# Optimization experiments

Hardware: AMD Instinct MI355X
Metric: run time of the kernel (lower is better)

Reference implementation:

```python
import jax, jax.numpy as jnp
import numpy as np

V, D, DI, DS, DC, DTR, L, H, BS, B, T = 32000, 512, 1024, 16, 4, 32, 4, 2048, 1024, 2, 1024


def layer_norm(x, g, b):
    m = jnp.mean(x, axis=-1, keepdims=True)
    v = jnp.mean(jnp.square(x - m), axis=-1, keepdims=True)
    return (x - m) * jax.lax.rsqrt(v + 1e-5) * g + b


def mamba(x, p):
    # x: [B, T, D]
    Bb = x.shape[0]
    xz = jnp.einsum('btd,ed->bte', x, p['W_in'])          # [B,T,2*DI]
    u, z = jnp.split(xz, 2, axis=-1)
    # causal depthwise conv over time
    uc = jnp.transpose(u, (0, 2, 1))                       # [B,DI,T]
    uc = jax.lax.conv_general_dilated(uc, p['conv_w'][:, None, :], (1,), [(DC - 1, 0)], feature_group_count=DI)
    uc = uc + p['conv_b'][None, :, None]
    u = jax.nn.silu(jnp.transpose(uc, (0, 2, 1)))          # [B,T,DI]
    x_dbl = jnp.einsum('btd,ed->bte', u, p['W_xp'])        # [B,T,DTR+2*DS]
    dt = jax.nn.softplus(jnp.einsum('btr,dr->btd', x_dbl[..., :DTR], p['W_dt']) + p['b_dt'])  # [B,T,DI]
    Bm = x_dbl[..., DTR:DTR + DS]                          # [B,T,DS]
    Cm = x_dbl[..., DTR + DS:]                             # [B,T,DS]
    A = -jnp.exp(p['A_log'])                               # [DI,DS]

    def step(h, inp):
        dt_t, B_t, C_t, u_t = inp                          # [B,DI],[B,DS],[B,DS],[B,DI]
        dA = jnp.exp(dt_t[:, :, None] * A)                 # [B,DI,DS]
        h = dA * h + (dt_t * u_t)[:, :, None] * B_t[:, None, :]
        return h, jnp.einsum('bds,bs->bd', h, C_t)

    h0 = jnp.zeros((Bb, DI, DS), x.dtype)
    _, ys = jax.lax.scan(step, h0, (dt.transpose(1, 0, 2), Bm.transpose(1, 0, 2), Cm.transpose(1, 0, 2), u.transpose(1, 0, 2)))
    y = ys.transpose(1, 0, 2) + u * p['D_p']               # skip term D*u
    y = y * jax.nn.silu(z)
    return jnp.einsum('bte,de->btd', y, p['W_out'])


def setup_inputs() -> dict:
    key = jax.random.key(0)
    ks = jax.random.split(key, 16)
    s = 0.02
    rn = lambda k, sh: (jax.random.normal(k, sh, jnp.float32) * s)
    inp = {
        'idx': jax.random.randint(ks[0], (B, T), 0, V),
        'tok_emb': rn(ks[1], (V, D)),
        'pos_emb': rn(ks[2], (BS, D)),
        'ln1_g': jnp.ones((L, D), jnp.float32), 'ln1_b': jnp.zeros((L, D), jnp.float32),
        'W_in': rn(ks[3], (L, 2 * DI, D)),
        'conv_w': rn(ks[4], (L, DI, DC)), 'conv_b': jnp.zeros((L, DI), jnp.float32),
        'W_xp': rn(ks[5], (L, DTR + 2 * DS, DI)),
        'W_dt': rn(ks[6], (L, DI, DTR)), 'b_dt': jnp.full((L, DI), -4.6, jnp.float32),
        'A_log': jnp.tile(jnp.log(jnp.arange(1, DS + 1, dtype=jnp.float32))[None, None, :], (L, DI, 1)),
        'D_p': jnp.ones((L, DI), jnp.float32),
        'W_out': rn(ks[7], (L, D, DI)),
        'ln2_g': jnp.ones((L, D), jnp.float32), 'ln2_b': jnp.zeros((L, D), jnp.float32),
        'W_f1': rn(ks[8], (L, H, D)), 'b_f1': jnp.zeros((L, H), jnp.float32),
        'W_f2': rn(ks[9], (L, D, H)), 'b_f2': jnp.zeros((L, D), jnp.float32),
        'lm_w': rn(ks[10], (V, D)), 'lm_b': jnp.zeros((V,), jnp.float32),
    }
    return inp


def reference(idx, tok_emb, pos_emb, ln1_g, ln1_b, W_in, conv_w, conv_b, W_xp, W_dt, b_dt, A_log, D_p, W_out, ln2_g, ln2_b, W_f1, b_f1, W_f2, b_f2, lm_w, lm_b):
    x = tok_emb[idx] + pos_emb[:idx.shape[1]]              # [B,T,D]
    layers = {'ln1_g': ln1_g, 'ln1_b': ln1_b, 'W_in': W_in, 'conv_w': conv_w, 'conv_b': conv_b,
              'W_xp': W_xp, 'W_dt': W_dt, 'b_dt': b_dt, 'A_log': A_log, 'D_p': D_p, 'W_out': W_out,
              'ln2_g': ln2_g, 'ln2_b': ln2_b, 'W_f1': W_f1, 'b_f1': b_f1, 'W_f2': W_f2, 'b_f2': b_f2}

    def blk(x, p):
        x = x + mamba(layer_norm(x, p['ln1_g'], p['ln1_b']), p)
        h = layer_norm(x, p['ln2_g'], p['ln2_b'])
        h = jax.nn.relu(jnp.einsum('btd,hd->bth', h, p['W_f1']) + p['b_f1'])
        x = x + jnp.einsum('bth,dh->btd', h, p['W_f2']) + p['b_f2']
        return x, None

    x, _ = jax.lax.scan(blk, x, layers)
    logits = jnp.einsum('btd,vd->btv', x, lm_w) + lm_b     # [B,T,V]
    return logits
```

## Files before the change

### kernel.cpp

```cpp
#include <hip/hip_runtime.h>
#include <cstdint>
#include <cstddef>

typedef __bf16 bf16;
typedef __bf16 bf16x8 __attribute__((ext_vector_type(8)));
typedef __bf16 bf16x4 __attribute__((ext_vector_type(4)));
typedef float  f32x4  __attribute__((ext_vector_type(4)));

#define D_MODEL 512
#define D_INNER 1024
#define D_STATE 16
#define D_CONV  4
#define DT_RANK 32
#define N_LAYER 4
#define H_FFN   2048
#define SEQ_T   1024
#define BATCH   2
#define BT      (BATCH * SEQ_T)
#define VOCAB   32000

#define NCHUNK  16
#define CHUNK   (SEQ_T / NCHUNK)

__device__ __forceinline__ float b2f(bf16 x) { return (float)x; }
__device__ __forceinline__ bf16  f2b(float x) { return (bf16)x; }

__device__ __forceinline__ float rdf(const void* p, long i, int bf) {
  return bf ? (float)((const bf16*)p)[i] : ((const float*)p)[i];
}

__device__ __forceinline__ void async16(const void* g, void* l) {
  __builtin_amdgcn_global_load_lds((const __attribute__((address_space(1))) void*)g,
                                   (__attribute__((address_space(3))) void*)l, 16, 0, 0);
}

__global__ void probe_k(const unsigned short* __restrict__ tok,
                        const unsigned short* __restrict__ pos,
                        int* __restrict__ flag)
{
  int lane = threadIdx.x;
  int bad = 0;
  for (int i = lane; i < 512; i += 64) {
    int e0 = (tok[i] >> 7) & 0xFF;
    int e1 = (pos[i] >> 7) & 0xFF;
    if (e0 >= 134 || e1 >= 134) bad = 1;
  }
  unsigned long long m = __ballot(bad);
  if (lane == 0) *flag = (m == 0ULL) ? 1 : 0;
}

__global__ __launch_bounds__(256) void cvt_k(const float4* __restrict__ src,
                                             bf16* __restrict__ dst,
                                             int n4, const int* __restrict__ dflag)
{
  if (*dflag) return;
  int i = blockIdx.x * 256 + threadIdx.x;
  if (i >= n4) return;
  float4 v = src[i];
  bf16x4 o; o[0] = f2b(v.x); o[1] = f2b(v.y); o[2] = f2b(v.z); o[3] = f2b(v.w);
  *(bf16x4*)(dst + (size_t)i * 4) = o;
}

template<int OUTMODE, bool RELU>
__global__ __launch_bounds__(256) void gemm_nt(
    const bf16* __restrict__ A, const bf16* __restrict__ Barena,
    const void* __restrict__ Braw, long boff,
    void* __restrict__ Cout, const void* __restrict__ bias, long biasoff,
    const float* __restrict__ res, const int* __restrict__ dflag,
    int M, int N, int K)
{
  __shared__ __attribute__((aligned(16))) bf16 As[128 * 32];
  __shared__ __attribute__((aligned(16))) bf16 Bs[128 * 32];

  const int bf = *dflag;
  const bf16* Bw = bf ? ((const bf16*)Braw + boff) : Barena;

  const int tid  = threadIdx.x;
  const int lane = tid & 63;
  const int q    = lane >> 4;
  const int m16  = lane & 15;
  const int w    = tid >> 6;
  const int wr   = w >> 1, wc = w & 1;

  const int rowA0 = blockIdx.y * 128;
  const int rowB0 = blockIdx.x * 128;

  f32x4 acc[4][4] = {};

  for (int k0 = 0; k0 < K; k0 += 32) {
#pragma unroll
    for (int r = 0; r < 2; r++) {
      int ci  = r * 256 + tid;
      int row = ci >> 2;
      int kc  = ci & 3;
      const bf16* ga = A  + (size_t)(rowA0 + row) * K + (k0 + kc * 8);
      const bf16* gb = Bw + (size_t)(rowB0 + row) * K + (k0 + kc * 8);
      char* la = (char*)As + (size_t)(r * 256 + (tid & 192)) * 16;
      char* lb = (char*)Bs + (size_t)(r * 256 + (tid & 192)) * 16;
      async16(ga, la);
      async16(gb, lb);
    }
    __syncthreads();

    bf16x8 af[4], bfr[4];
#pragma unroll
    for (int mt = 0; mt < 4; mt++)
      af[mt] = *(const bf16x8*)&As[(wr * 64 + mt * 16 + m16) * 32 + q * 8];
#pragma unroll
    for (int nt = 0; nt < 4; nt++)
      bfr[nt] = *(const bf16x8*)&Bs[(wc * 64 + nt * 16 + m16) * 32 + q * 8];

#pragma unroll
    for (int mt = 0; mt < 4; mt++)
#pragma unroll
      for (int nt = 0; nt < 4; nt++)
        acc[mt][nt] = __builtin_amdgcn_mfma_f32_16x16x32_bf16(
            af[mt], bfr[nt], acc[mt][nt], 0, 0, 0);

    __syncthreads();
  }

#pragma unroll
  for (int mt = 0; mt < 4; mt++) {
#pragma unroll
    for (int r = 0; r < 4; r++) {
      int row = rowA0 + wr * 64 + mt * 16 + q * 4 + r;
#pragma unroll
      for (int nt = 0; nt < 4; nt++) {
        int col = rowB0 + wc * 64 + nt * 16 + m16;
        float v = acc[mt][nt][r];
        if (bias) v += rdf(bias, biasoff + col, bf);
        if (res)  v += res[(size_t)row * N + col];
        if (RELU) v = fmaxf(v, 0.f);
        size_t oi = (size_t)row * N + col;
        if (OUTMODE == 1 || (OUTMODE == 2 && bf)) ((bf16*)Cout)[oi] = f2b(v);
        else                                      ((float*)Cout)[oi] = v;
      }
    }
  }
}

__global__ void embed_k(const int* __restrict__ idx, const void* __restrict__ tok,
                        const void* __restrict__ pos, float* __restrict__ x,
                        const int* __restrict__ dflag)
{
  int bf = *dflag;
  int bt = blockIdx.x;
  int t  = bt & (SEQ_T - 1);
  long rowv = idx[bt];
  for (int i = threadIdx.x; i < D_MODEL; i += blockDim.x)
    x[(size_t)bt * D_MODEL + i] = rdf(tok, rowv * D_MODEL + i, bf)
                                + rdf(pos, (long)t * D_MODEL + i, bf);
}

__global__ __launch_bounds__(64) void ln_k(const float* __restrict__ x,
                                           const void* __restrict__ g,
                                           const void* __restrict__ bb,
                                           long goff,
                                           bf16* __restrict__ out,
                                           const int* __restrict__ dflag)
{
  int bf = *dflag;
  int row = blockIdx.x;
  const float4* xr = (const float4*)(x + (size_t)row * D_MODEL);
  int l = threadIdx.x;
  float4 v0 = xr[l];
  float4 v1 = xr[64 + l];
  float s  = (v0.x + v0.y) + (v0.z + v0.w) + (v1.x + v1.y) + (v1.z + v1.w);
  float ss = v0.x*v0.x + v0.y*v0.y + v0.z*v0.z + v0.w*v0.w
           + v1.x*v1.x + v1.y*v1.y + v1.z*v1.z + v1.w*v1.w;
#pragma unroll
  for (int o = 32; o; o >>= 1) { s += __shfl_xor(s, o); ss += __shfl_xor(ss, o); }
  float m   = s  * (1.f / 512.f);
  float var = ss * (1.f / 512.f) - m * m;
  float inv = rsqrtf(var + 1e-5f);
  float vs[8] = {v0.x, v0.y, v0.z, v0.w, v1.x, v1.y, v1.z, v1.w};
  int i0 = l * 4, i1 = 256 + l * 4;
#pragma unroll
  for (int e = 0; e < 4; e++) {
    out[(size_t)row * D_MODEL + i0 + e] =
        f2b((vs[e] - m) * inv * rdf(g, goff + i0 + e, bf) + rdf(bb, goff + i0 + e, bf));
    out[(size_t)row * D_MODEL + i1 + e] =
        f2b((vs[4 + e] - m) * inv * rdf(g, goff + i1 + e, bf) + rdf(bb, goff + i1 + e, bf));
  }
}

__global__ __launch_bounds__(256) void conv_silu_k(const float* __restrict__ xz,
                                                   const void* __restrict__ cw,
                                                   const void* __restrict__ cb,
                                                   long cwoff, long cboff,
                                                   bf16* __restrict__ u,
                                                   const int* __restrict__ dflag)
{
  int bf  = *dflag;
  int gid = blockIdx.x * 256 + threadIdx.x;
  int d   = gid & (D_INNER - 1);
  int bt  = gid >> 10;
  int t   = bt & (SEQ_T - 1);
  float acc = rdf(cb, cboff + d, bf);
#pragma unroll
  for (int k = 0; k < D_CONV; k++) {
    int tt = t + k - (D_CONV - 1);
    if (tt >= 0)
      acc += xz[(size_t)(bt + k - (D_CONV - 1)) * (2 * D_INNER) + d]
           * rdf(cw, cwoff + (long)d * D_CONV + k, bf);
  }
  float sig = 1.f / (1.f + __expf(-acc));
  u[gid] = f2b(acc * sig);
}

__global__ __launch_bounds__(256) void xdbl_k(const bf16* __restrict__ u,
                                              const bf16* __restrict__ Warena,
                                              const void* __restrict__ Wraw, long woff,
                                              float* __restrict__ xd,
                                              const int* __restrict__ dflag)
{
  int bf = *dflag;
  const bf16* Wxp = bf ? ((const bf16*)Wraw + woff) : Warena;
  int t = blockIdx.x;
  __shared__ float us[D_INNER];
  __shared__ float red[256];
  for (int i = threadIdx.x; i < D_INNER; i += 256)
    us[i] = b2f(u[(size_t)t * D_INNER + i]);
  __syncthreads();
  int j = threadIdx.x >> 2, p = threadIdx.x & 3;
  const bf16x8* wr = (const bf16x8*)(Wxp + (size_t)j * D_INNER + p * 256);
  float s = 0.f;
#pragma unroll 4
  for (int c = 0; c < 32; c++) {
    bf16x8 wv = wr[c];
    int k = p * 256 + c * 8;
#pragma unroll
    for (int e = 0; e < 8; e++) s += us[k + e] * b2f(wv[e]);
  }
  red[threadIdx.x] = s;
  __syncthreads();
  if (p == 0)
    xd[(size_t)t * 64 + j] = red[threadIdx.x] + red[threadIdx.x + 1]
                           + red[threadIdx.x + 2] + red[threadIdx.x + 3];
}

__global__ __launch_bounds__(256) void dt_k(const float* __restrict__ xd,
                                            const bf16* __restrict__ Warena,
                                            const void* __restrict__ Wraw, long woff,
                                            const void* __restrict__ bdt, long boff,
                                            float* __restrict__ dtb,
                                            const int* __restrict__ dflag)
{
  int bf = *dflag;
  const bf16* Wdt = bf ? ((const bf16*)Wraw + woff) : Warena;
  int t = blockIdx.x >> 2;
  int d = ((blockIdx.x & 3) << 8) + threadIdx.x;
  __shared__ float xr[DT_RANK];
  if (threadIdx.x < DT_RANK) xr[threadIdx.x] = xd[(size_t)t * 64 + threadIdx.x];
  __syncthreads();
  float s = rdf(bdt, boff + d, bf);
  const bf16x8* wr = (const bf16x8*)(Wdt + (size_t)d * DT_RANK);
#pragma unroll
  for (int c = 0; c < 4; c++) {
    bf16x8 wv = wr[c];
#pragma unroll
    for (int e = 0; e < 8; e++) s += xr[c * 8 + e] * b2f(wv[e]);
  }
  s = (s > 20.f) ? s : log1pf(__expf(s));
  dtb[(size_t)t * D_INNER + d] = s;
}

__global__ __launch_bounds__(256) void scanA_k(const float* __restrict__ dtb,
                                               const bf16* __restrict__ u,
                                               const float* __restrict__ xd,
                                               const void* __restrict__ A_log, long aoff,
                                               float* __restrict__ Pb,
                                               float* __restrict__ Qb,
                                               const int* __restrict__ dflag)
{
  int bf = *dflag;
  int s  = threadIdx.x & 15;
  int dl = threadIdx.x >> 4;
  int c  = blockIdx.x & (NCHUNK - 1);
  int dg = (blockIdx.x >> 4) & 63;
  int b  = blockIdx.x >> 10;
  int d  = dg * 16 + dl;

  float Av = -__expf(rdf(A_log, aoff + (long)d * D_STATE + s, bf));
  float h = 0.f, P = 1.f;
  size_t row0 = (size_t)b * SEQ_T + (size_t)c * CHUNK;

  float dt_n = dtb[row0 * D_INNER + d];
  float u_n  = b2f(u[row0 * D_INNER + d]);
  float B_n  = xd[row0 * 64 + DT_RANK + s];

  for (int t = 0; t < CHUNK; t++) {
    float dt_v = dt_n, u_v = u_n, Bv = B_n;
    if (t + 1 < CHUNK) {
      size_t r1 = row0 + t + 1;
      dt_n = dtb[r1 * D_INNER + d];
      u_n  = b2f(u[r1 * D_INNER + d]);
      B_n  = xd[r1 * 64 + DT_RANK + s];
    }
    float dA = __expf(dt_v * Av);
    P *= dA;
    h = dA * h + (dt_v * u_v) * Bv;
  }
  size_t o = (((size_t)b * D_INNER + d) * D_STATE + s) * NCHUNK + c;
  Pb[o] = P;
  Qb[o] = h;
}

__global__ __launch_bounds__(256) void scanB_k(const float* __restrict__ Pb,
                                               const float* __restrict__ Qb,
                                               float* __restrict__ Hin)
{
  int tid = blockIdx.x * 256 + threadIdx.x;
  size_t base = (size_t)tid * NCHUNK;
  float h = 0.f;
#pragma unroll
  for (int c = 0; c < NCHUNK; c++) {
    Hin[base + c] = h;
    h = Pb[base + c] * h + Qb[base + c];
  }
}

__global__ __launch_bounds__(256) void scanC_k(const float* __restrict__ dtb,
                                               const bf16* __restrict__ u,
                                               const float* __restrict__ xd,
                                               const float* __restrict__ xz,
                                               const void* __restrict__ A_log, long aoff,
                                               const void* __restrict__ D_p, long doff,
                                               const float* __restrict__ Hin,
                                               bf16* __restrict__ y,
                                               const int* __restrict__ dflag)
{
  int bf = *dflag;
  int s  = threadIdx.x & 15;
  int dl = threadIdx.x >> 4;
  int c  = blockIdx.x & (NCHUNK - 1);
  int dg = (blockIdx.x >> 4) & 63;
  int b  = blockIdx.x >> 10;
  int d  = dg * 16 + dl;

  float Av = -__expf(rdf(A_log, aoff + (long)d * D_STATE + s, bf));
  float Dv = rdf(D_p, doff + d, bf);
  float h  = Hin[(((size_t)b * D_INNER + d) * D_STATE + s) * NCHUNK + c];
  size_t row0 = (size_t)b * SEQ_T + (size_t)c * CHUNK;

  float dt_n = dtb[row0 * D_INNER + d];
  float u_n  = b2f(u[row0 * D_INNER + d]);
  float B_n  = xd[row0 * 64 + DT_RANK + s];
  float C_n  = xd[row0 * 64 + DT_RANK + D_STATE + s];

  for (int t = 0; t < CHUNK; t++) {
    float dt_v = dt_n, u_v = u_n, Bv = B_n, Cv = C_n;
    if (t + 1 < CHUNK) {
      size_t r1 = row0 + t + 1;
      dt_n = dtb[r1 * D_INNER + d];
      u_n  = b2f(u[r1 * D_INNER + d]);
      B_n  = xd[r1 * 64 + DT_RANK + s];
      C_n  = xd[r1 * 64 + DT_RANK + D_STATE + s];
    }
    float dA = __expf(dt_v * Av);
    h = dA * h + (dt_v * u_v) * Bv;
    float p = h * Cv;
    p += __shfl_xor(p, 1);
    p += __shfl_xor(p, 2);
    p += __shfl_xor(p, 4);
    p += __shfl_xor(p, 8);
    if (s == 0) {
      size_t r = row0 + t;
      float zv  = xz[r * (2 * D_INNER) + D_INNER + d];
      float sig = 1.f / (1.f + __expf(-zv));
      y[r * D_INNER + d] = f2b((p + u_v * Dv) * (zv * sig));
    }
  }
}

__global__ void cast_k(const float* __restrict__ x, bf16* __restrict__ o, int n)
{
  int i = blockIdx.x * 256 + threadIdx.x;
  if (i < n) o[i] = f2b(x[i]);
}

extern "C" void kernel_launch(void* const* d_in, const int* in_sizes, int n_in,
                              void* d_out, int out_size, void* d_ws, size_t ws_size,
                              hipStream_t stream)
{
  const int* idx = (const int*)d_in[0];
  const void* tok    = d_in[1];
  const void* pos    = d_in[2];
  const void* ln1_g  = d_in[3];
  const void* ln1_b  = d_in[4];
  const void* W_in   = d_in[5];
  const void* conv_w = d_in[6];
  const void* conv_b = d_in[7];
  const void* W_xp   = d_in[8];
  const void* W_dt   = d_in[9];
  const void* b_dt   = d_in[10];
  const void* A_log  = d_in[11];
  const void* D_p    = d_in[12];
  const void* W_out  = d_in[13];
  const void* ln2_g  = d_in[14];
  const void* ln2_b  = d_in[15];
  const void* W_f1   = d_in[16];
  const void* b_f1   = d_in[17];
  const void* W_f2   = d_in[18];
  const void* b_f2   = d_in[19];
  const void* lm_w   = d_in[20];
  const void* lm_b   = d_in[21];

  char* ws = (char*)d_ws;
  int*  dflag = (int*)ws;    ws += 256;
  float* x_res = (float*)ws; ws += (size_t)BT * D_MODEL * 4;
  float* xz    = (float*)ws; ws += (size_t)BT * 2 * D_INNER * 4;
  float* xdbl  = (float*)ws; ws += (size_t)BT * 64 * 4;
  float* dtb   = (float*)ws; ws += (size_t)BT * D_INNER * 4;
  bf16* lnbuf  = (bf16*)ws;  ws += (size_t)BT * D_MODEL * 2;
  bf16* ubuf   = (bf16*)ws;  ws += (size_t)BT * D_INNER * 2;
  bf16* ybuf   = (bf16*)ws;  ws += (size_t)BT * D_INNER * 2;
  bf16* hbuf   = (bf16*)ws;  ws += (size_t)BT * H_FFN * 2;
  float* Pbuf  = (float*)ws; ws += (size_t)BATCH * D_INNER * D_STATE * NCHUNK * 4;
  float* Qbuf  = (float*)ws; ws += (size_t)BATCH * D_INNER * D_STATE * NCHUNK * 4;
  float* Hin   = (float*)ws; ws += (size_t)BATCH * D_INNER * D_STATE * NCHUNK * 4;
  bf16* aW_in  = (bf16*)ws;  ws += (size_t)N_LAYER * 2*D_INNER * D_MODEL * 2;
  bf16* aW_xp  = (bf16*)ws;  ws += (size_t)N_LAYER * 64 * D_INNER * 2;
  bf16* aW_dt  = (bf16*)ws;  ws += (size_t)N_LAYER * D_INNER * DT_RANK * 2;
  bf16* aW_out = (bf16*)ws;  ws += (size_t)N_LAYER * D_MODEL * D_INNER * 2;
  bf16* aW_f1  = (bf16*)ws;  ws += (size_t)N_LAYER * H_FFN * D_MODEL * 2;
  bf16* aW_f2  = (bf16*)ws;  ws += (size_t)N_LAYER * D_MODEL * H_FFN * 2;
  bf16* aLm    = (bf16*)ws;  ws += (size_t)VOCAB * D_MODEL * 2;

  probe_k<<<1, 64, 0, stream>>>((const unsigned short*)tok,
                                (const unsigned short*)pos, dflag);

  auto cvt = [&](const void* src, bf16* dst, long n) {
    int n4 = (int)(n / 4);
    cvt_k<<<(n4 + 255) / 256, 256, 0, stream>>>((const float4*)src, dst, n4, dflag);
  };
  cvt(W_in,  aW_in,  (long)N_LAYER * 2*D_INNER * D_MODEL);
  cvt(W_xp,  aW_xp,  (long)N_LAYER * 64 * D_INNER);
  cvt(W_dt,  aW_dt,  (long)N_LAYER * D_INNER * DT_RANK);
  cvt(W_out, aW_out, (long)N_LAYER * D_MODEL * D_INNER);
  cvt(W_f1,  aW_f1,  (long)N_LAYER * H_FFN * D_MODEL);
  cvt(W_f2,  aW_f2,  (long)N_LAYER * D_MODEL * H_FFN);
  cvt(lm_w,  aLm,    (long)VOCAB * D_MODEL);

  embed_k<<<BT, 256, 0, stream>>>(idx, tok, pos, x_res, dflag);

  for (int l = 0; l < N_LAYER; l++) {
    long oWin = (long)l * 2*D_INNER * D_MODEL;
    long oWxp = (long)l * 64 * D_INNER;
    long oWdt = (long)l * D_INNER * DT_RANK;
    long oWo  = (long)l * D_MODEL * D_INNER;
    long oWf1 = (long)l * H_FFN * D_MODEL;
    long oWf2 = (long)l * D_MODEL * H_FFN;
    long oA   = (long)l * D_INNER * D_STATE;
    long oD   = (long)l * D_INNER;

    ln_k<<<BT, 64, 0, stream>>>(x_res, ln1_g, ln1_b, (long)l * D_MODEL, lnbuf, dflag);

    gemm_nt<0, false><<<dim3(2 * D_INNER / 128, BT / 128), 256, 0, stream>>>(
        lnbuf, aW_in + oWin, W_in, oWin, xz, nullptr, 0, nullptr, dflag,
        BT, 2 * D_INNER, D_MODEL);

    conv_silu_k<<<BT * D_INNER / 256, 256, 0, stream>>>(
        xz, conv_w, conv_b, (long)l * D_INNER * D_CONV, oD, ubuf, dflag);

    xdbl_k<<<BT, 256, 0, stream>>>(ubuf, aW_xp + oWxp, W_xp, oWxp, xdbl, dflag);

    dt_k<<<BT * 4, 256, 0, stream>>>(
        xdbl, aW_dt + oWdt, W_dt, oWdt, b_dt, oD, dtb, dflag);

    scanA_k<<<BATCH * 64 * NCHUNK, 256, 0, stream>>>(
        dtb, ubuf, xdbl, A_log, oA, Pbuf, Qbuf, dflag);
    scanB_k<<<BATCH * D_INNER * D_STATE / 256, 256, 0, stream>>>(Pbuf, Qbuf, Hin);
    scanC_k<<<BATCH * 64 * NCHUNK, 256, 0, stream>>>(
        dtb, ubuf, xdbl, xz, A_log, oA, D_p, oD, Hin, ybuf, dflag);

    gemm_nt<0, false><<<dim3(D_MODEL / 128, BT / 128), 256, 0, stream>>>(
        ybuf, aW_out + oWo, W_out, oWo, x_res, nullptr, 0, x_res, dflag,
        BT, D_MODEL, D_INNER);

    ln_k<<<BT, 64, 0, stream>>>(x_res, ln2_g, ln2_b, (long)l * D_MODEL, lnbuf, dflag);

    gemm_nt<1, true><<<dim3(H_FFN / 128, BT / 128), 256, 0, stream>>>(
        lnbuf, aW_f1 + oWf1, W_f1, oWf1, hbuf, b_f1, (long)l * H_FFN, nullptr, dflag,
        BT, H_FFN, D_MODEL);

    gemm_nt<0, false><<<dim3(D_MODEL / 128, BT / 128), 256, 0, stream>>>(
        hbuf, aW_f2 + oWf2, W_f2, oWf2, x_res, b_f2, (long)l * D_MODEL, x_res, dflag,
        BT, D_MODEL, H_FFN);
  }

  cast_k<<<BT * D_MODEL / 256, 256, 0, stream>>>(x_res, lnbuf, BT * D_MODEL);

  gemm_nt<2, false><<<dim3(VOCAB / 128, BT / 128), 256, 0, stream>>>(
      lnbuf, aLm, lm_w, 0, d_out, lm_b, 0, nullptr, dflag,
      BT, VOCAB, D_MODEL);
}
```

Before: 1.760 ms.

## Triple-buffer GEMM K-loop, swizzle LM-head blocks, vectorize xdbl input load

The GEMM main loop moves from one LDS tile per step to a 3-slot ring. Loads are issued two tiles ahead, and vmcnt/lgkmcnt waits with raw barriers replace __syncthreads, so global-to-LDS copies overlap the MFMA work. The LM-head GEMM also remaps block IDs so that consecutive blocks share the same N tile, which is meant to improve L2 reuse of lm_w. In xdbl_k the u row is loaded with 8-wide vector loads. The extra slots triple LDS use and may lower occupancy, and the hand-written wait counts must match the number of async loads per stage. The wraparound prefetch in the final iterations reloads tiles that are never used.

```diff
diff --git a/kernel.cpp b/kernel.cpp
--- a/kernel.cpp
+++ b/kernel.cpp
@@ -61,7 +61,7 @@
   *(bf16x4*)(dst + (size_t)i * 4) = o;
 }
 
-template<int OUTMODE, bool RELU>
+template<int OUTMODE, bool RELU, bool SWZ>
 __global__ __launch_bounds__(256) void gemm_nt(
     const bf16* __restrict__ A, const bf16* __restrict__ Barena,
     const void* __restrict__ Braw, long boff,
@@ -69,8 +69,8 @@
     const float* __restrict__ res, const int* __restrict__ dflag,
     int M, int N, int K)
 {
-  __shared__ __attribute__((aligned(16))) bf16 As[128 * 32];
-  __shared__ __attribute__((aligned(16))) bf16 Bs[128 * 32];
+  __shared__ __attribute__((aligned(16))) bf16 As[3][128 * 32];
+  __shared__ __attribute__((aligned(16))) bf16 Bs[3][128 * 32];
 
   const int bf = *dflag;
   const bf16* Bw = bf ? ((const bf16*)Braw + boff) : Barena;
@@ -82,12 +82,27 @@
   const int w    = tid >> 6;
   const int wr   = w >> 1, wc = w & 1;
 
-  const int rowA0 = blockIdx.y * 128;
-  const int rowB0 = blockIdx.x * 128;
+  int bx = blockIdx.x, by = blockIdx.y;
+  if (SWZ) {
+    int gx = gridDim.x, gy = gridDim.y;
+    int n  = gx * gy;
+    if ((n & 7) == 0) {
+      int id  = by * gx + bx;
+      int nid = (id & 7) * (n >> 3) + (id >> 3);
+      bx = nid / gy;
+      by = nid % gy;
+    }
+  }
+
+  const int rowA0 = by * 128;
+  const int rowB0 = bx * 128;
 
   f32x4 acc[4][4] = {};
 
-  for (int k0 = 0; k0 < K; k0 += 32) {
+  const int NT = K >> 5;
+
+  auto stage = [&](int slot, int kt) {
+    int k0 = kt << 5;
 #pragma unroll
     for (int r = 0; r < 2; r++) {
       int ci  = r * 256 + tid;
@@ -95,20 +110,35 @@
       int kc  = ci & 3;
       const bf16* ga = A  + (size_t)(rowA0 + row) * K + (k0 + kc * 8);
       const bf16* gb = Bw + (size_t)(rowB0 + row) * K + (k0 + kc * 8);
-      char* la = (char*)As + (size_t)(r * 256 + (tid & 192)) * 16;
-      char* lb = (char*)Bs + (size_t)(r * 256 + (tid & 192)) * 16;
+      char* la = (char*)&As[slot][0] + (size_t)(r * 256 + (tid & 192)) * 16;
+      char* lb = (char*)&Bs[slot][0] + (size_t)(r * 256 + (tid & 192)) * 16;
       async16(ga, la);
       async16(gb, lb);
     }
-    __syncthreads();
-
+  };
+
+  stage(0, 0);
+  stage(1, 1 < NT ? 1 : 0);
+
+  for (int t = 0; t < NT; t++) {
+    int t2 = t + 2; if (t2 >= NT) t2 -= NT;
+    stage((t + 2) % 3, t2);
+
+    asm volatile("s_waitcnt vmcnt(8)" ::: "memory");
+    __builtin_amdgcn_s_barrier();
+
+    const int sl = t % 3;
     bf16x8 af[4], bfr[4];
 #pragma unroll
     for (int mt = 0; mt < 4; mt++)
-      af[mt] = *(const bf16x8*)&As[(wr * 64 + mt * 16 + m16) * 32 + q * 8];
+      af[mt] = *(const bf16x8*)&As[sl][(wr * 64 + mt * 16 + m16) * 32 + q * 8];
 #pragma unroll
     for (int nt = 0; nt < 4; nt++)
-      bfr[nt] = *(const bf16x8*)&Bs[(wc * 64 + nt * 16 + m16) * 32 + q * 8];
+      bfr[nt] = *(const bf16x8*)&Bs[sl][(wc * 64 + nt * 16 + m16) * 32 + q * 8];
+
+    asm volatile("s_waitcnt lgkmcnt(0)" ::: "memory");
+    __builtin_amdgcn_sched_barrier(0);
+    __builtin_amdgcn_s_barrier();
 
 #pragma unroll
     for (int mt = 0; mt < 4; mt++)
@@ -116,9 +146,9 @@
       for (int nt = 0; nt < 4; nt++)
         acc[mt][nt] = __builtin_amdgcn_mfma_f32_16x16x32_bf16(
             af[mt], bfr[nt], acc[mt][nt], 0, 0, 0);
-
-    __syncthreads();
-  }
+  }
+
+  asm volatile("s_waitcnt vmcnt(0)" ::: "memory");
 
 #pragma unroll
   for (int mt = 0; mt < 4; mt++) {
@@ -220,8 +250,11 @@
   int t = blockIdx.x;
   __shared__ float us[D_INNER];
   __shared__ float red[256];
-  for (int i = threadIdx.x; i < D_INNER; i += 256)
-    us[i] = b2f(u[(size_t)t * D_INNER + i]);
+  if (threadIdx.x < D_INNER / 8) {
+    bf16x8 v = *(const bf16x8*)(u + (size_t)t * D_INNER + threadIdx.x * 8);
+#pragma unroll
+    for (int e = 0; e < 8; e++) us[threadIdx.x * 8 + e] = b2f(v[e]);
+  }
   __syncthreads();
   int j = threadIdx.x >> 2, p = threadIdx.x & 3;
   const bf16x8* wr = (const bf16x8*)(Wxp + (size_t)j * D_INNER + p * 256);
@@ -457,7 +490,7 @@
 
     ln_k<<<BT, 64, 0, stream>>>(x_res, ln1_g, ln1_b, (long)l * D_MODEL, lnbuf, dflag);
 
-    gemm_nt<0, false><<<dim3(2 * D_INNER / 128, BT / 128), 256, 0, stream>>>(
+    gemm_nt<0, false, false><<<dim3(2 * D_INNER / 128, BT / 128), 256, 0, stream>>>(
         lnbuf, aW_in + oWin, W_in, oWin, xz, nullptr, 0, nullptr, dflag,
         BT, 2 * D_INNER, D_MODEL);
 
@@ -475,24 +508,24 @@
     scanC_k<<<BATCH * 64 * NCHUNK, 256, 0, stream>>>(
         dtb, ubuf, xdbl, xz, A_log, oA, D_p, oD, Hin, ybuf, dflag);
 
-    gemm_nt<0, false><<<dim3(D_MODEL / 128, BT / 128), 256, 0, stream>>>(
+    gemm_nt<0, false, false><<<dim3(D_MODEL / 128, BT / 128), 256, 0, stream>>>(
         ybuf, aW_out + oWo, W_out, oWo, x_res, nullptr, 0, x_res, dflag,
         BT, D_MODEL, D_INNER);
 
     ln_k<<<BT, 64, 0, stream>>>(x_res, ln2_g, ln2_b, (long)l * D_MODEL, lnbuf, dflag);
 
-    gemm_nt<1, true><<<dim3(H_FFN / 128, BT / 128), 256, 0, stream>>>(
+    gemm_nt<1, true, false><<<dim3(H_FFN / 128, BT / 128), 256, 0, stream>>>(
         lnbuf, aW_f1 + oWf1, W_f1, oWf1, hbuf, b_f1, (long)l * H_FFN, nullptr, dflag,
         BT, H_FFN, D_MODEL);
 
-    gemm_nt<0, false><<<dim3(D_MODEL / 128, BT / 128), 256, 0, stream>>>(
+    gemm_nt<0, false, false><<<dim3(D_MODEL / 128, BT / 128), 256, 0, stream>>>(
         hbuf, aW_f2 + oWf2, W_f2, oWf2, x_res, b_f2, (long)l * D_MODEL, x_res, dflag,
         BT, D_MODEL, H_FFN);
   }
 
   cast_k<<<BT * D_MODEL / 256, 256, 0, stream>>>(x_res, lnbuf, BT * D_MODEL);
 
-  gemm_nt<2, false><<<dim3(VOCAB / 128, BT / 128), 256, 0, stream>>>(
+  gemm_nt<2, false, true><<<dim3(VOCAB / 128, BT / 128), 256, 0, stream>>>(
       lnbuf, aLm, lm_w, 0, d_out, lm_b, 0, nullptr, dflag,
       BT, VOCAB, D_MODEL);
 }
```

Measured after the change: 1.840 ms. 1.05x slower.

## Split-K the narrow residual GEMMs and swizzle the LM-head GEMM grid

Applied to the files above, without the earlier changes.

The out-projection and FFN2 GEMMs (N=512) only launched 64 workgroups. They now run a 4-way split-K kernel that writes fp32 partial sums, followed by a vectorized reduction kernel that adds bias and residual. This spreads the work across far more CUs, at the cost of extra partial-buffer traffic and one more launch per GEMM. The LM-head GEMM is split into two column halves with a block-index swizzle for cache locality, and the xdbl kernel loads its input row as vectors of 8 bf16.

```diff
diff --git a/kernel.cpp b/kernel.cpp
--- a/kernel.cpp
+++ b/kernel.cpp
@@ -22,6 +22,8 @@
 #define NCHUNK  16
 #define CHUNK   (SEQ_T / NCHUNK)
 
+#define KSPLIT  4
+
 __device__ __forceinline__ float b2f(bf16 x) { return (float)x; }
 __device__ __forceinline__ bf16  f2b(float x) { return (bf16)x; }
 
@@ -61,13 +63,13 @@
   *(bf16x4*)(dst + (size_t)i * 4) = o;
 }
 
-template<int OUTMODE, bool RELU>
+template<int OUTMODE, bool RELU, bool SWZ>
 __global__ __launch_bounds__(256) void gemm_nt(
     const bf16* __restrict__ A, const bf16* __restrict__ Barena,
     const void* __restrict__ Braw, long boff,
     void* __restrict__ Cout, const void* __restrict__ bias, long biasoff,
     const float* __restrict__ res, const int* __restrict__ dflag,
-    int M, int N, int K)
+    int M, int N, int K, int ldc, int col0)
 {
   __shared__ __attribute__((aligned(16))) bf16 As[128 * 32];
   __shared__ __attribute__((aligned(16))) bf16 Bs[128 * 32];
@@ -82,8 +84,20 @@
   const int w    = tid >> 6;
   const int wr   = w >> 1, wc = w & 1;
 
-  const int rowA0 = blockIdx.y * 128;
-  const int rowB0 = blockIdx.x * 128;
+  int bx = blockIdx.x, by = blockIdx.y;
+  if (SWZ) {
+    int gx = gridDim.x, gy = gridDim.y;
+    int n  = gx * gy;
+    if ((n & 7) == 0) {
+      int id  = by * gx + bx;
+      int nid = (id & 7) * (n >> 3) + (id >> 3);
+      bx = nid / gy;
+      by = nid % gy;
+    }
+  }
+
+  const int rowA0 = by * 128;
+  const int rowB0 = bx * 128;
 
   f32x4 acc[4][4] = {};
 
@@ -127,17 +141,120 @@
       int row = rowA0 + wr * 64 + mt * 16 + q * 4 + r;
 #pragma unroll
       for (int nt = 0; nt < 4; nt++) {
-        int col = rowB0 + wc * 64 + nt * 16 + m16;
+        int col = col0 + rowB0 + wc * 64 + nt * 16 + m16;
         float v = acc[mt][nt][r];
         if (bias) v += rdf(bias, biasoff + col, bf);
-        if (res)  v += res[(size_t)row * N + col];
+        if (res)  v += res[(size_t)row * ldc + col];
         if (RELU) v = fmaxf(v, 0.f);
-        size_t oi = (size_t)row * N + col;
+        size_t oi = (size_t)row * ldc + col;
         if (OUTMODE == 1 || (OUTMODE == 2 && bf)) ((bf16*)Cout)[oi] = f2b(v);
         else                                      ((float*)Cout)[oi] = v;
       }
     }
   }
+}
+
+__global__ __launch_bounds__(256) void gemm_nt_sk(
+    const bf16* __restrict__ A, const bf16* __restrict__ Barena,
+    const void* __restrict__ Braw, long boff,
+    float* __restrict__ Cpart, const int* __restrict__ dflag,
+    int M, int N, int K)
+{
+  __shared__ __attribute__((aligned(16))) bf16 As[128 * 32];
+  __shared__ __attribute__((aligned(16))) bf16 Bs[128 * 32];
+
+  const int bf = *dflag;
+  const bf16* Bw = bf ? ((const bf16*)Braw + boff) : Barena;
+
+  const int tid  = threadIdx.x;
+  const int lane = tid & 63;
+  const int q    = lane >> 4;
+  const int m16  = lane & 15;
+  const int w    = tid >> 6;
+  const int wr   = w >> 1, wc = w & 1;
+
+  const int rowA0 = blockIdx.y * 128;
+  const int rowB0 = blockIdx.x * 128;
+  const int ks    = blockIdx.z;
+  const int kBeg  = ks * (K / KSPLIT);
+  const int kEnd  = kBeg + (K / KSPLIT);
+
+  f32x4 acc[4][4] = {};
+
+  for (int k0 = kBeg; k0 < kEnd; k0 += 32) {
+#pragma unroll
+    for (int r = 0; r < 2; r++) {
+      int ci  = r * 256 + tid;
+      int row = ci >> 2;
+      int kc  = ci & 3;
+      const bf16* ga = A  + (size_t)(rowA0 + row) * K + (k0 + kc * 8);
+      const bf16* gb = Bw + (size_t)(rowB0 + row) * K + (k0 + kc * 8);
+      char* la = (char*)As + (size_t)(r * 256 + (tid & 192)) * 16;
+      char* lb = (char*)Bs + (size_t)(r * 256 + (tid & 192)) * 16;
+      async16(ga, la);
+      async16(gb, lb);
+    }
+    __syncthreads();
+
+    bf16x8 af[4], bfr[4];
+#pragma unroll
+    for (int mt = 0; mt < 4; mt++)
+      af[mt] = *(const bf16x8*)&As[(wr * 64 + mt * 16 + m16) * 32 + q * 8];
+#pragma unroll
+    for (int nt = 0; nt < 4; nt++)
+      bfr[nt] = *(const bf16x8*)&Bs[(wc * 64 + nt * 16 + m16) * 32 + q * 8];
+
+#pragma unroll
+    for (int mt = 0; mt < 4; mt++)
+#pragma unroll
+      for (int nt = 0; nt < 4; nt++)
+        acc[mt][nt] = __builtin_amdgcn_mfma_f32_16x16x32_bf16(
+            af[mt], bfr[nt], acc[mt][nt], 0, 0, 0);
+
+    __syncthreads();
+  }
+
+#pragma unroll
+  for (int mt = 0; mt < 4; mt++) {
+#pragma unroll
+    for (int r = 0; r < 4; r++) {
+      int row = rowA0 + wr * 64 + mt * 16 + q * 4 + r;
+#pragma unroll
+      for (int nt = 0; nt < 4; nt++) {
+        int col = rowB0 + wc * 64 + nt * 16 + m16;
+        Cpart[((size_t)ks * M + row) * N + col] = acc[mt][nt][r];
+      }
+    }
+  }
+}
+
+__global__ __launch_bounds__(256) void redk_k(const float* __restrict__ part,
+                                              const void* __restrict__ bias, long biasoff,
+                                              const float* __restrict__ res,
+                                              float* __restrict__ out,
+                                              int n, int N, const int* __restrict__ dflag)
+{
+  int bf = *dflag;
+  int i = blockIdx.x * 256 + threadIdx.x;
+  if (i >= n) return;
+  f32x4 s = ((const f32x4*)part)[i];
+#pragma unroll
+  for (int ks = 1; ks < KSPLIT; ks++) {
+    f32x4 p = ((const f32x4*)part)[(size_t)ks * n + i];
+    s.x += p.x; s.y += p.y; s.z += p.z; s.w += p.w;
+  }
+  if (bias) {
+    int col = (i * 4) & (N - 1);
+    s.x += rdf(bias, biasoff + col,     bf);
+    s.y += rdf(bias, biasoff + col + 1, bf);
+    s.z += rdf(bias, biasoff + col + 2, bf);
+    s.w += rdf(bias, biasoff + col + 3, bf);
+  }
+  if (res) {
+    f32x4 r = ((const f32x4*)res)[i];
+    s.x += r.x; s.y += r.y; s.z += r.z; s.w += r.w;
+  }
+  ((f32x4*)out)[i] = s;
 }
 
 __global__ void embed_k(const int* __restrict__ idx, const void* __restrict__ tok,
@@ -220,8 +337,11 @@
   int t = blockIdx.x;
   __shared__ float us[D_INNER];
   __shared__ float red[256];
-  for (int i = threadIdx.x; i < D_INNER; i += 256)
-    us[i] = b2f(u[(size_t)t * D_INNER + i]);
+  if (threadIdx.x < D_INNER / 8) {
+    bf16x8 v = *(const bf16x8*)(u + (size_t)t * D_INNER + threadIdx.x * 8);
+#pragma unroll
+    for (int e = 0; e < 8; e++) us[threadIdx.x * 8 + e] = b2f(v[e]);
+  }
   __syncthreads();
   int j = threadIdx.x >> 2, p = threadIdx.x & 3;
   const bf16x8* wr = (const bf16x8*)(Wxp + (size_t)j * D_INNER + p * 256);
@@ -417,6 +537,7 @@
   bf16* ubuf   = (bf16*)ws;  ws += (size_t)BT * D_INNER * 2;
   bf16* ybuf   = (bf16*)ws;  ws += (size_t)BT * D_INNER * 2;
   bf16* hbuf   = (bf16*)ws;  ws += (size_t)BT * H_FFN * 2;
+  float* cpart = (float*)ws; ws += (size_t)KSPLIT * BT * D_MODEL * 4;
   float* Pbuf  = (float*)ws; ws += (size_t)BATCH * D_INNER * D_STATE * NCHUNK * 4;
   float* Qbuf  = (float*)ws; ws += (size_t)BATCH * D_INNER * D_STATE * NCHUNK * 4;
   float* Hin   = (float*)ws; ws += (size_t)BATCH * D_INNER * D_STATE * NCHUNK * 4;
@@ -457,9 +578,9 @@
 
     ln_k<<<BT, 64, 0, stream>>>(x_res, ln1_g, ln1_b, (long)l * D_MODEL, lnbuf, dflag);
 
-    gemm_nt<0, false><<<dim3(2 * D_INNER / 128, BT / 128), 256, 0, stream>>>(
+    gemm_nt<0, false, false><<<dim3(2 * D_INNER / 128, BT / 128), 256, 0, stream>>>(
         lnbuf, aW_in + oWin, W_in, oWin, xz, nullptr, 0, nullptr, dflag,
-        BT, 2 * D_INNER, D_MODEL);
+        BT, 2 * D_INNER, D_MODEL, 2 * D_INNER, 0);
 
     conv_silu_k<<<BT * D_INNER / 256, 256, 0, stream>>>(
         xz, conv_w, conv_b, (long)l * D_INNER * D_CONV, oD, ubuf, dflag);
@@ -475,24 +596,30 @@
     scanC_k<<<BATCH * 64 * NCHUNK, 256, 0, stream>>>(
         dtb, ubuf, xdbl, xz, A_log, oA, D_p, oD, Hin, ybuf, dflag);
 
-    gemm_nt<0, false><<<dim3(D_MODEL / 128, BT / 128), 256, 0, stream>>>(
-        ybuf, aW_out + oWo, W_out, oWo, x_res, nullptr, 0, x_res, dflag,
-        BT, D_MODEL, D_INNER);
+    gemm_nt_sk<<<dim3(D_MODEL / 128, BT / 128, KSPLIT), 256, 0, stream>>>(
+        ybuf, aW_out + oWo, W_out, oWo, cpart, dflag, BT, D_MODEL, D_INNER);
+    redk_k<<<(BT * D_MODEL / 4 + 255) / 256, 256, 0, stream>>>(
+        cpart, nullptr, 0, x_res, x_res, BT * D_MODEL / 4, D_MODEL, dflag);
 
     ln_k<<<BT, 64, 0, stream>>>(x_res, ln2_g, ln2_b, (long)l * D_MODEL, lnbuf, dflag);
 
-    gemm_nt<1, true><<<dim3(H_FFN / 128, BT / 128), 256, 0, stream>>>(
+    gemm_nt<1, true, false><<<dim3(H_FFN / 128, BT / 128), 256, 0, stream>>>(
         lnbuf, aW_f1 + oWf1, W_f1, oWf1, hbuf, b_f1, (long)l * H_FFN, nullptr, dflag,
-        BT, H_FFN, D_MODEL);
-
-    gemm_nt<0, false><<<dim3(D_MODEL / 128, BT / 128), 256, 0, stream>>>(
-        hbuf, aW_f2 + oWf2, W_f2, oWf2, x_res, b_f2, (long)l * D_MODEL, x_res, dflag,
-        BT, D_MODEL, H_FFN);
+        BT, H_FFN, D_MODEL, H_FFN, 0);
+
+    gemm_nt_sk<<<dim3(D_MODEL / 128, BT / 128, KSPLIT), 256, 0, stream>>>(
+        hbuf, aW_f2 + oWf2, W_f2, oWf2, cpart, dflag, BT, D_MODEL, H_FFN);
+    redk_k<<<(BT * D_MODEL / 4 + 255) / 256, 256, 0, stream>>>(
+        cpart, b_f2, (long)l * D_MODEL, x_res, x_res, BT * D_MODEL / 4, D_MODEL, dflag);
   }
 
   cast_k<<<BT * D_MODEL / 256, 256, 0, stream>>>(x_res, lnbuf, BT * D_MODEL);
 
-  gemm_nt<2, false><<<dim3(VOCAB / 128, BT / 128), 256, 0, stream>>>(
-      lnbuf, aLm, lm_w, 0, d_out, lm_b, 0, nullptr, dflag,
-      BT, VOCAB, D_MODEL);
-}
+  for (int h = 0; h < 2; h++) {
+    int colbase = h * (VOCAB / 2);
+    gemm_nt<2, false, true><<<dim3(VOCAB / 2 / 128, BT / 128), 256, 0, stream>>>(
+        lnbuf, aLm + (size_t)colbase * D_MODEL, lm_w, (long)colbase * D_MODEL,
+        d_out, lm_b, 0, nullptr, dflag,
+        BT, VOCAB / 2, D_MODEL, VOCAB, colbase);
+  }
+}
```

Measured after the change: 1.501 ms. 14.7% less time.
